# Kernel tuning notes

Hardware: AMD Instinct MI355X
Metric: run time of the kernel (lower is better)

The kernel has to match this reference:

```python
import jax, jax.numpy as jnp
import numpy as np

TEMP = 0.07  # module hardcodes self.temp = 0.07 regardless of ctor arg
N, C = 8192, 256


def setup_inputs() -> dict:
    key = jax.random.key(0)
    kq, kk = jax.random.split(key)
    q = jax.random.normal(kq, (N, C), dtype=jnp.float32)
    k = jax.random.normal(kk, (N, C), dtype=jnp.float32)
    return {"q": q, "k": k}


def reference(q, k):
    # Original builds logits = [l_pos, l_neg_row] per sample i where
    # l_pos = q_i . k_i and l_neg_row = q_i . k_j for j != i, then applies
    # CrossEntropyLoss with label 0. That logits row is exactly a permutation
    # of the full similarity row sim[i, :] = q_i @ k.T (diagonal = positive),
    # so CE(logits/T, 0) == logsumexp(sim_i/T) - sim_ii/T. Single fused GEMM
    # + row-wise logsumexp, identical math and gradients.
    sim = jnp.matmul(q, k.T) / TEMP            # [N, N]
    pos = jnp.diagonal(sim)                    # [N]
    lse = jax.nn.logsumexp(sim, axis=1)        # [N]
    return jnp.mean(lse - pos)                 # scalar loss
```

## Files before the change

kernel.cpp:

```cpp
#include <hip/hip_runtime.h>
#include <stdint.h>


#define N_ROWS 8192
#define C_DIM  256
#define BN     64
#define SPLIT  8
#define JCOLS  (N_ROWS / SPLIT)
#define JTILES (JCOLS / BN)
#define BLK_ROWS 128

typedef __attribute__((ext_vector_type(8)))  _Float16 half8;
typedef __attribute__((ext_vector_type(4)))  _Float16 half4;
typedef __attribute__((ext_vector_type(16))) float    f32x16;

#if __has_builtin(__builtin_amdgcn_exp2f)
#define EXP2(x) __builtin_amdgcn_exp2f(x)
#else
#define EXP2(x) exp2f(x)
#endif
#if __has_builtin(__builtin_amdgcn_logf)
#define LOG2(x) __builtin_amdgcn_logf(x)
#else
#define LOG2(x) log2f(x)
#endif

__device__ __forceinline__ void gload_lds16(const void* g, void* l) {
  __builtin_amdgcn_global_load_lds(
      (const __attribute__((address_space(1))) unsigned int*)g,
      (__attribute__((address_space(3))) unsigned int*)l, 16, 0, 0);
}

__global__ void cvt_kernel(const float* __restrict__ q, const float* __restrict__ k,
                           _Float16* __restrict__ qh, _Float16* __restrict__ kh,
                           float* __restrict__ pP) {
  const float QS = 20.60992915555663f;
  int i = blockIdx.x * 256 + threadIdx.x;
  float4 qv = ((const float4*)q)[i];
  float4 kv = ((const float4*)k)[i];
  half4 qo, ko;
  qo[0] = (_Float16)(qv.x * QS); qo[1] = (_Float16)(qv.y * QS);
  qo[2] = (_Float16)(qv.z * QS); qo[3] = (_Float16)(qv.w * QS);
  ko[0] = (_Float16)kv.x; ko[1] = (_Float16)kv.y;
  ko[2] = (_Float16)kv.z; ko[3] = (_Float16)kv.w;
  ((half4*)qh)[i] = qo;
  ((half4*)kh)[i] = ko;

  float d = (float)qo[0] * (float)ko[0];
  d = fmaf((float)qo[1], (float)ko[1], d);
  d = fmaf((float)qo[2], (float)ko[2], d);
  d = fmaf((float)qo[3], (float)ko[3], d);
#pragma unroll
  for (int off = 1; off < 64; off <<= 1) d += __shfl_xor(d, off);
  if ((threadIdx.x & 63) == 0) pP[i >> 6] = d;
}

__launch_bounds__(256, 2)
__global__ void sim_lse_kernel(const _Float16* __restrict__ qh,
                               const _Float16* __restrict__ kh,
                               float* __restrict__ pM,
                               float* __restrict__ pS) {
  __shared__ __align__(16) _Float16 kt[2 * BN * C_DIM];
  const int tid  = threadIdx.x;
  const int lane = tid & 63;
  const int wave = tid >> 6;
  const int r    = lane & 31;
  const int hi   = lane >> 5;

  const int bid  = blockIdx.x;
  const int sp   = bid & (SPLIT - 1);
  const int rb   = bid >> 3;
  const int row0 = rb * BLK_ROWS + wave * 32;

  half8 a[16];
  {
    const _Float16* qr = qh + (size_t)(row0 + r) * C_DIM + hi * 8;
#pragma unroll
    for (int ks = 0; ks < 16; ++ks) a[ks] = *(const half8*)(qr + ks * 16);
  }

  float M[16], S[16];
#pragma unroll
  for (int j = 0; j < 16; ++j) { M[j] = -__builtin_inff(); S[j] = 0.f; }

  const int bb0 = r * 512 + ((hi ^ r) << 4);
  const int bb1 = bb0 + 32 * 512;

  const char* ksrc = (const char*)(kh + (size_t)sp * JCOLS * C_DIM);
  char* lds = (char*)kt;

#pragma unroll
  for (int it = 0; it < 8; ++it) {
    int linear = it * 4096 + tid * 16;
    int row = linear >> 9;
    int gc  = ((linear >> 4) & 31) ^ (row & 31);
    gload_lds16(ksrc + row * 512 + gc * 16, lds + linear);
  }

  for (int jt = 0; jt < JTILES; ++jt) {
    __syncthreads();
    const char* cur = lds + (jt & 1) * 32768;

    if (jt + 1 < JTILES) {
      const char* src = ksrc + (size_t)(jt + 1) * (BN * C_DIM * 2);
      char* nxt = lds + ((jt + 1) & 1) * 32768;
#pragma unroll
      for (int it = 0; it < 8; ++it) {
        int linear = it * 4096 + tid * 16;
        int row = linear >> 9;
        int gc  = ((linear >> 4) & 31) ^ (row & 31);
        gload_lds16(src + row * 512 + gc * 16, nxt + linear);
      }
    }

    f32x16 acc0, acc1;
#pragma unroll
    for (int j = 0; j < 16; ++j) { acc0[j] = 0.f; acc1[j] = 0.f; }

#pragma unroll
    for (int ks = 0; ks < 16; ++ks) {
      half8 b0 = *(const half8*)(cur + (bb0 ^ (ks * 32)));
      half8 b1 = *(const half8*)(cur + (bb1 ^ (ks * 32)));
      acc0 = __builtin_amdgcn_mfma_f32_32x32x16_f16(a[ks], b0, acc0, 0, 0, 0);
      acc1 = __builtin_amdgcn_mfma_f32_32x32x16_f16(a[ks], b1, acc1, 0, 0, 0);
    }

#pragma unroll
    for (int j = 0; j < 16; ++j) {
      float v0 = acc0[j], v1 = acc1[j];
      float tmax  = fmaxf(v0, v1);
      float newM  = fmaxf(M[j], tmax);
      float alpha = EXP2(M[j] - newM);
      float p = EXP2(v0 - newM) + EXP2(v1 - newM);
      S[j] = fmaf(S[j], alpha, p);
      M[j] = newM;
    }
  }

#pragma unroll
  for (int j = 0; j < 16; ++j) {
#pragma unroll
    for (int off = 1; off < 32; off <<= 1) {
      float Mo = __shfl_xor(M[j], off);
      float So = __shfl_xor(S[j], off);
      float nm = fmaxf(M[j], Mo);
      S[j] = S[j] * EXP2(M[j] - nm) + So * EXP2(Mo - nm);
      M[j] = nm;
    }
  }

  if ((lane & 31) == 0) {
#pragma unroll
    for (int j = 0; j < 16; ++j) {
      int grow = row0 + (j & 3) + 8 * (j >> 2) + 4 * hi;
      pM[(size_t)sp * N_ROWS + grow] = M[j];
      pS[(size_t)sp * N_ROWS + grow] = S[j];
    }
  }
}

__global__ void finish1_kernel(const float* __restrict__ pM, const float* __restrict__ pS,
                               const float* __restrict__ pP, float* __restrict__ pPart) {
  const int tid = threadIdx.x;
  const int r = blockIdx.x * 256 + tid;
  float m = -__builtin_inff();
#pragma unroll
  for (int s = 0; s < SPLIT; ++s) m = fmaxf(m, pM[s * N_ROWS + r]);
  float ssum = 0.f;
#pragma unroll
  for (int s = 0; s < SPLIT; ++s)
    ssum = fmaf(pS[s * N_ROWS + r], EXP2(pM[s * N_ROWS + r] - m), ssum);
  float accl = (m + LOG2(ssum)) - pP[r];
#pragma unroll
  for (int off = 1; off < 64; off <<= 1) accl += __shfl_xor(accl, off);
  __shared__ float wsum[4];
  if ((tid & 63) == 0) wsum[tid >> 6] = accl;
  __syncthreads();
  if (tid == 0)
    pPart[blockIdx.x] = wsum[0] + wsum[1] + wsum[2] + wsum[3];
}

__global__ void finish2_kernel(const float* __restrict__ pPart, float* __restrict__ out) {
  const int tid = threadIdx.x;
  float v = (tid < 32) ? pPart[tid] : 0.f;
#pragma unroll
  for (int off = 1; off < 64; off <<= 1) v += __shfl_xor(v, off);
  if (tid == 0)
    out[0] = v * (0.69314718055994531f / (float)N_ROWS);
}

extern "C" void kernel_launch(void* const* d_in, const int* in_sizes, int n_in,
                              void* d_out, int out_size, void* d_ws, size_t ws_size,
                              hipStream_t stream) {
  const float* q = (const float*)d_in[0];
  const float* k = (const float*)d_in[1];
  float* out = (float*)d_out;
  char* ws = (char*)d_ws;

  _Float16* qh = (_Float16*)ws;
  _Float16* kh = (_Float16*)(ws + (size_t)N_ROWS * C_DIM * 2);
  float* pM = (float*)(ws + (size_t)N_ROWS * C_DIM * 4);
  float* pS = pM + SPLIT * N_ROWS;
  float* pP = pS + SPLIT * N_ROWS;
  float* pPart = pP + N_ROWS;

  cvt_kernel<<<dim3(N_ROWS * C_DIM / 4 / 256), dim3(256), 0, stream>>>(q, k, qh, kh, pP);
  sim_lse_kernel<<<dim3((N_ROWS / BLK_ROWS) * SPLIT), dim3(256), 0, stream>>>(qh, kh, pM, pS);
  finish1_kernel<<<dim3(N_ROWS / 256), dim3(256), 0, stream>>>(pM, pS, pP, pPart);
  finish2_kernel<<<dim3(1), dim3(64), 0, stream>>>(pPart, out);
}
```

Before: 116.0 us.

## Halve K tile width, double split count and raise occupancy to four blocks

Shrinks the per-iteration K tile from 64 to 32 columns, so each wave keeps one MFMA accumulator instead of two and the LDS double buffer drops to 32 KB. The split across columns grows from 8 to 16, doubling the grid, and launch bounds now request 4 blocks per CU for more latency hiding. The cost is an online-softmax rescale (an extra exp per element) for every 32 columns instead of every 64, fewer MFMAs between barriers, and twice as many partial max/sum values to merge.

```diff
diff --git a/kernel.cpp b/kernel.cpp
--- a/kernel.cpp
+++ b/kernel.cpp
@@ -4,11 +4,12 @@
 
 #define N_ROWS 8192
 #define C_DIM  256
-#define BN     64
-#define SPLIT  8
+#define BN     32
+#define SPLIT  16
 #define JCOLS  (N_ROWS / SPLIT)
 #define JTILES (JCOLS / BN)
 #define BLK_ROWS 128
+#define TILE_B  (BN * C_DIM * 2)
 
 typedef __attribute__((ext_vector_type(8)))  _Float16 half8;
 typedef __attribute__((ext_vector_type(4)))  _Float16 half4;
@@ -55,7 +56,7 @@
   if ((threadIdx.x & 63) == 0) pP[i >> 6] = d;
 }
 
-__launch_bounds__(256, 2)
+__launch_bounds__(256, 4)
 __global__ void sim_lse_kernel(const _Float16* __restrict__ qh,
                                const _Float16* __restrict__ kh,
                                float* __restrict__ pM,
@@ -69,7 +70,7 @@
 
   const int bid  = blockIdx.x;
   const int sp   = bid & (SPLIT - 1);
-  const int rb   = bid >> 3;
+  const int rb   = bid >> 4;
   const int row0 = rb * BLK_ROWS + wave * 32;
 
   half8 a[16];
@@ -83,55 +84,51 @@
 #pragma unroll
   for (int j = 0; j < 16; ++j) { M[j] = -__builtin_inff(); S[j] = 0.f; }
 
-  const int bb0 = r * 512 + ((hi ^ r) << 4);
-  const int bb1 = bb0 + 32 * 512;
+  const int bb = r * 512 + ((hi ^ r) << 4);
 
   const char* ksrc = (const char*)(kh + (size_t)sp * JCOLS * C_DIM);
   char* lds = (char*)kt;
 
 #pragma unroll
-  for (int it = 0; it < 8; ++it) {
+  for (int it = 0; it < 4; ++it) {
     int linear = it * 4096 + tid * 16;
     int row = linear >> 9;
-    int gc  = ((linear >> 4) & 31) ^ (row & 31);
+    int gc  = ((linear >> 4) & 31) ^ row;
     gload_lds16(ksrc + row * 512 + gc * 16, lds + linear);
   }
 
   for (int jt = 0; jt < JTILES; ++jt) {
     __syncthreads();
-    const char* cur = lds + (jt & 1) * 32768;
+    const char* cur = lds + (jt & 1) * TILE_B;
 
     if (jt + 1 < JTILES) {
-      const char* src = ksrc + (size_t)(jt + 1) * (BN * C_DIM * 2);
-      char* nxt = lds + ((jt + 1) & 1) * 32768;
-#pragma unroll
-      for (int it = 0; it < 8; ++it) {
+      const char* src = ksrc + (size_t)(jt + 1) * TILE_B;
+      char* nxt = lds + ((jt + 1) & 1) * TILE_B;
+#pragma unroll
+      for (int it = 0; it < 4; ++it) {
         int linear = it * 4096 + tid * 16;
         int row = linear >> 9;
-        int gc  = ((linear >> 4) & 31) ^ (row & 31);
+        int gc  = ((linear >> 4) & 31) ^ row;
         gload_lds16(src + row * 512 + gc * 16, nxt + linear);
       }
     }
 
-    f32x16 acc0, acc1;
-#pragma unroll
-    for (int j = 0; j < 16; ++j) { acc0[j] = 0.f; acc1[j] = 0.f; }
+    f32x16 acc;
+#pragma unroll
+    for (int j = 0; j < 16; ++j) acc[j] = 0.f;
 
 #pragma unroll
     for (int ks = 0; ks < 16; ++ks) {
-      half8 b0 = *(const half8*)(cur + (bb0 ^ (ks * 32)));
-      half8 b1 = *(const half8*)(cur + (bb1 ^ (ks * 32)));
-      acc0 = __builtin_amdgcn_mfma_f32_32x32x16_f16(a[ks], b0, acc0, 0, 0, 0);
-      acc1 = __builtin_amdgcn_mfma_f32_32x32x16_f16(a[ks], b1, acc1, 0, 0, 0);
+      half8 b = *(const half8*)(cur + (bb ^ (ks * 32)));
+      acc = __builtin_amdgcn_mfma_f32_32x32x16_f16(a[ks], b, acc, 0, 0, 0);
     }
 
 #pragma unroll
     for (int j = 0; j < 16; ++j) {
-      float v0 = acc0[j], v1 = acc1[j];
-      float tmax  = fmaxf(v0, v1);
-      float newM  = fmaxf(M[j], tmax);
+      float v = acc[j];
+      float newM  = fmaxf(M[j], v);
       float alpha = EXP2(M[j] - newM);
-      float p = EXP2(v0 - newM) + EXP2(v1 - newM);
+      float p     = EXP2(v - newM);
       S[j] = fmaf(S[j], alpha, p);
       M[j] = newM;
     }
```

New measurement: 139.5 us. 20.2% more time.
